# Kernel tuning notes

Measured on AMD Instinct MI355X. Metric: run time of the kernel, lower is better.

## Reference

```python
import jax, jax.numpy as jnp
import numpy as np

D = 1024
H = 16
B = 4
S = 2048
NEG = -1000000000.0


def setup_inputs() -> dict:
    key = jax.random.key(0)
    ks = jax.random.split(key, 12)
    s = 0.02
    inp = {
        "Q": jax.random.normal(ks[0], (B, S, D), jnp.float32),
        "K": jax.random.normal(ks[1], (B, S, D), jnp.float32),
        "V": jax.random.normal(ks[2], (B, S, D), jnp.float32),
        # causal mask, broadcastable to [B, H, S, S]
        "mask": jnp.broadcast_to(jnp.tril(jnp.ones((S, S), bool)), (B, 1, S, S)),
        "Wq": jax.random.normal(ks[3], (D, D), jnp.float32) * s,
        "bq": jnp.zeros((D,), jnp.float32),
        "Wk": jax.random.normal(ks[4], (D, D), jnp.float32) * s,
        "bk": jnp.zeros((D,), jnp.float32),
        "Wv": jax.random.normal(ks[5], (D, D), jnp.float32) * s,
        "bv": jnp.zeros((D,), jnp.float32),
        "Wo": jax.random.normal(ks[6], (D, D), jnp.float32) * s,
        "bo": jnp.zeros((D,), jnp.float32),
    }
    return inp


def reference(Q, K, V, mask, Wq, bq, Wk, bk, Wv, bv, Wo, bo):
    d = D // H  # head dim
    def split(x):  # [B,S,D] -> [B,H,S,d]
        Bx, Sx, _ = x.shape
        return x.reshape(Bx, Sx, H, d).transpose(0, 2, 1, 3)

    q = split(Q @ Wq + bq)
    k = split(K @ Wk + bk)
    v = split(V @ Wv + bv)

    scores = jnp.einsum("bhsd,bhtd->bhst", q, k) / jnp.sqrt(jnp.float32(d))
    scores = jnp.where(mask, scores, NEG)
    attn = jax.nn.softmax(scores, axis=-1)
    out = jnp.einsum("bhst,bhtd->bhsd", attn, v)  # [B,H,S,d]
    out = out.transpose(0, 2, 1, 3).reshape(Q.shape[0], Q.shape[1], D)
    return out @ Wo + bo
```

## Files before the change

kernel.cpp:

```cpp
#include <hip/hip_runtime.h>
#include <hip/hip_bf16.h>
#include <type_traits>

#define DEV __device__ __forceinline__

typedef short bf16x8 __attribute__((ext_vector_type(8)));
typedef float f32x4 __attribute__((ext_vector_type(4)));
typedef float f32x16 __attribute__((ext_vector_type(16)));
typedef unsigned u32x4 __attribute__((ext_vector_type(4)));

static DEV unsigned short f2bf(float f) {
  unsigned u = __builtin_bit_cast(unsigned, f);
  u += 0x7FFFu + ((u >> 16) & 1u);
  return (unsigned short)(u >> 16);
}

static DEV unsigned cvtpk(float lo, float hi) {
  unsigned d;
  asm("v_cvt_pk_bf16_f32 %0, %1, %2" : "=v"(d) : "v"(lo), "v"(hi));
  return d;
}

static DEV void pl32(unsigned& x, unsigned& y) {
  asm("v_permlane32_swap_b32 %0, %1" : "+v"(x), "+v"(y));
}

static DEV float vmax3(float a, float b, float c) {
  float d;
  asm("v_max3_f32 %0, %1, %2, %3" : "=v"(d) : "v"(a), "v"(b), "v"(c));
  return d;
}

static DEV void gl_lds16(const unsigned short* g, unsigned short* l) {
  __builtin_amdgcn_global_load_lds(
      (const __attribute__((address_space(1))) unsigned*)g,
      (__attribute__((address_space(3))) unsigned*)l, 16, 0, 0);
}

#define QSCALE 0.18033688f

__global__ __launch_bounds__(256) void wtrans4(const float* __restrict__ W0,
                                               const float* __restrict__ W1,
                                               const float* __restrict__ W2,
                                               const float* __restrict__ W3,
                                               unsigned short* __restrict__ T0,
                                               unsigned short* __restrict__ T1,
                                               unsigned short* __restrict__ T2,
                                               unsigned short* __restrict__ T3) {
  const int z = blockIdx.z;
  const float* W = z == 0 ? W0 : z == 1 ? W1 : z == 2 ? W2 : W3;
  unsigned short* Wt = z == 0 ? T0 : z == 1 ? T1 : z == 2 ? T2 : T3;
  const float wsc = (z == 0) ? QSCALE : 1.0f;
  __shared__ __align__(16) unsigned short T[64][72];
  const int tid = threadIdx.x;
  const int k0 = blockIdx.x * 64, n0 = blockIdx.y * 64;
  const int r = tid >> 4, c4 = (tid & 15) * 4;
  for (int j = 0; j < 4; ++j) {
    int row = j * 16 + r;
    float4 v = *(const float4*)&W[(size_t)(k0 + row) * 1024 + n0 + c4];
    ushort4 w;
    w.x = f2bf(v.x * wsc); w.y = f2bf(v.y * wsc);
    w.z = f2bf(v.z * wsc); w.w = f2bf(v.w * wsc);
    *(ushort4*)&T[row][c4] = w;
  }
  __syncthreads();
  for (int j = 0; j < 4; ++j) {
    int n = j * 16 + r;
    ushort4 w;
    w.x = T[c4 + 0][n]; w.y = T[c4 + 1][n]; w.z = T[c4 + 2][n]; w.w = T[c4 + 3][n];
    *(ushort4*)&Wt[(size_t)(n0 + n) * 1024 + k0 + c4] = w;
  }
}

__global__ __launch_bounds__(256) void xcvt3(const float* __restrict__ S0,
                                             const float* __restrict__ S1,
                                             const float* __restrict__ S2,
                                             unsigned short* __restrict__ D0,
                                             unsigned short* __restrict__ D1,
                                             unsigned short* __restrict__ D2) {
  const int z = blockIdx.z;
  const float* S = z == 0 ? S0 : z == 1 ? S1 : S2;
  unsigned short* D = z == 0 ? D0 : z == 1 ? D1 : D2;
  const size_t stride = (size_t)gridDim.x * 256 * 8;
  for (size_t i = ((size_t)blockIdx.x * 256 + threadIdx.x) * 8; i < 8u * 1024 * 1024;
       i += stride) {
    float4 a = *(const float4*)&S[i];
    float4 b = *(const float4*)&S[i + 4];
    uint4 w;
    w.x = cvtpk(a.x, a.y);
    w.y = cvtpk(a.z, a.w);
    w.z = cvtpk(b.x, b.y);
    w.w = cvtpk(b.z, b.w);
    *(uint4*)&D[i] = w;
  }
}

template <typename OutT>
DEV void gemm_lds_body(const unsigned short* __restrict__ X,
                       const unsigned short* __restrict__ Wt,
                       const float* __restrict__ bias, OutT* __restrict__ Y,
                       float bsc) {
  __shared__ __align__(16) unsigned short As[128 * 64];
  __shared__ __align__(16) unsigned short Bs[128 * 64];
  const int tid = threadIdx.x, lane = tid & 63, wid = tid >> 6;
  const int m0 = blockIdx.x * 128, n0 = blockIdx.y * 128;
  const int wm = (wid >> 1) * 64, wn = (wid & 1) * 64;
  f32x4 acc[4][4] = {};

  const int srow = wid * 32 + (lane >> 3);
  const int scol = (((lane & 7) ^ ((lane >> 3) & 7))) * 8;
  const unsigned short* gA = &X[(size_t)(m0 + srow) * 1024 + scol];
  const unsigned short* gB = &Wt[(size_t)(n0 + srow) * 1024 + scol];
  unsigned short* lA = &As[wid * 32 * 64];
  unsigned short* lB = &Bs[wid * 32 * 64];

  for (int k0 = 0; k0 < 1024; k0 += 64) {
    __syncthreads();
#pragma unroll
    for (int j = 0; j < 4; ++j) {
      gl_lds16(gA + (size_t)j * 8 * 1024 + k0, lA + j * 8 * 64);
      gl_lds16(gB + (size_t)j * 8 * 1024 + k0, lB + j * 8 * 64);
    }
    __syncthreads();
#pragma unroll
    for (int kk = 0; kk < 2; ++kk) {
      const int kb = ((kk * 4 + (lane >> 4)) ^ (lane & 7)) * 8;
      bf16x8 af[4], bfr[4];
#pragma unroll
      for (int i = 0; i < 4; ++i)
        af[i] = *(const bf16x8*)&As[(wm + i * 16 + (lane & 15)) * 64 + kb];
#pragma unroll
      for (int i = 0; i < 4; ++i)
        bfr[i] = *(const bf16x8*)&Bs[(wn + i * 16 + (lane & 15)) * 64 + kb];
      __builtin_amdgcn_s_setprio(1);
#pragma unroll
      for (int mi = 0; mi < 4; ++mi)
#pragma unroll
        for (int ni = 0; ni < 4; ++ni)
          acc[mi][ni] =
              __builtin_amdgcn_mfma_f32_16x16x32_bf16(af[mi], bfr[ni], acc[mi][ni], 0, 0, 0);
      __builtin_amdgcn_s_setprio(0);
    }
  }
  for (int ni = 0; ni < 4; ++ni) {
    const int col = n0 + wn + ni * 16 + (lane & 15);
    const float bv = bias[col] * bsc;
    for (int mi = 0; mi < 4; ++mi) {
      const int row = m0 + wm + mi * 16 + (lane >> 4) * 4;
      for (int r = 0; r < 4; ++r) {
        float v = acc[mi][ni][r] + bv;
        if constexpr (std::is_same_v<OutT, float>)
          Y[(size_t)(row + r) * 1024 + col] = v;
        else
          Y[(size_t)(row + r) * 1024 + col] = f2bf(v);
      }
    }
  }
}

__global__ __launch_bounds__(256) void gemm_qkv3(
    const unsigned short* __restrict__ X0, const unsigned short* __restrict__ X1,
    const unsigned short* __restrict__ X2, const unsigned short* __restrict__ W0,
    const unsigned short* __restrict__ W1, const unsigned short* __restrict__ W2,
    const float* __restrict__ b0, const float* __restrict__ b1,
    const float* __restrict__ b2, unsigned short* __restrict__ Y0,
    unsigned short* __restrict__ Y1, unsigned short* __restrict__ Y2) {
  const int z = blockIdx.z;
  const unsigned short* X = z == 0 ? X0 : z == 1 ? X1 : X2;
  const unsigned short* Wt = z == 0 ? W0 : z == 1 ? W1 : W2;
  const float* bias = z == 0 ? b0 : z == 1 ? b1 : b2;
  unsigned short* Y = z == 0 ? Y0 : z == 1 ? Y1 : Y2;
  gemm_lds_body<unsigned short>(X, Wt, bias, Y, z == 0 ? QSCALE : 1.0f);
}

__global__ __launch_bounds__(256) void gemm_out(const unsigned short* __restrict__ X,
                                                const unsigned short* __restrict__ Wt,
                                                const float* __restrict__ bias,
                                                float* __restrict__ Y) {
  gemm_lds_body<float>(X, Wt, bias, Y, 1.0f);
}

__global__ __launch_bounds__(256) void vtrans(const unsigned short* __restrict__ vbf,
                                              unsigned short* __restrict__ vt) {
  __shared__ __align__(16) unsigned short T[64][72];
  const int tid = threadIdx.x;
  const int s0 = blockIdx.x * 64;
  const int bh = blockIdx.y, b = bh >> 4, h = bh & 15;
  const int col0 = h * 64;
  const int rr = tid >> 3, c8 = (tid & 7) * 8;
  for (int p = 0; p < 2; ++p) {
    const int row = rr + 32 * p;
    *(uint4*)&T[row][c8] =
        *(const uint4*)&vbf[((size_t)b * 2048 + s0 + row) * 1024 + col0 + c8];
  }
  __syncthreads();
  const int dv = tid & 63, ss = (tid >> 6) * 16;
  union { uint4 v[2]; unsigned short s[16]; } o;
#pragma unroll
  for (int i = 0; i < 16; ++i) o.s[i] = T[ss + i][dv];
  *(uint4*)&vt[((size_t)bh * 64 + dv) * 2048 + s0 + ss] = o.v[0];
  *(uint4*)&vt[((size_t)bh * 64 + dv) * 2048 + s0 + ss + 8] = o.v[1];
}

__global__ __launch_bounds__(256) void attn_fwd(const unsigned short* __restrict__ Qb,
                                                const unsigned short* __restrict__ Kb,
                                                const unsigned short* __restrict__ Vt,
                                                unsigned short* __restrict__ Ob) {
  constexpr int KP = 72;
  __shared__ __align__(16) unsigned short SM[4 * 64 * KP];
  const int tid = threadIdx.x, lane = tid & 63, wid = tid >> 6;
  const int l31 = lane & 31, hi = lane >> 5;
  const int id = blockIdx.x;
  const int xcd = id & 7, idx = id >> 3;
  const int bh = xcd + 8 * (idx & 7);
  const int qb = idx >> 3;
  const int q0 = (15 - qb) * 128;
  const int b = bh >> 4, h = bh & 15;
  const size_t rowbase = (size_t)b * 2048;
  const int col0 = h * 64;
  const int qmin = q0 + wid * 32;
  const int myq = qmin + l31;
  const unsigned short* Vrow = Vt + (size_t)bh * 64 * 2048;
  const int rr = tid >> 3, c8 = (tid & 7) * 8;

  bf16x8 qf[4];
#pragma unroll
  for (int c = 0; c < 4; ++c)
    qf[c] = *(const bf16x8*)&Qb[(rowbase + myq) * 1024 + col0 + c * 16 + hi * 8];

  const bf16x8 onesv =
      __builtin_bit_cast(bf16x8, (u32x4){0x3F803F80u, 0x3F803F80u, 0x3F803F80u, 0x3F803F80u});

  f32x16 o[2], rsa;
  o[0] = 0.f; o[1] = 0.f; rsa = 0.f;
  float mrow = -1.0e30f;

  const int NT = q0 / 64 + 2;
  uint4 kr0, kr1, vr0, vr1;
#define LOADT(KV0)                                                              \
  do {                                                                          \
    const int _k = (KV0);                                                       \
    kr0 = *(const uint4*)&Kb[(rowbase + _k + rr) * 1024 + col0 + c8];           \
    kr1 = *(const uint4*)&Kb[(rowbase + _k + rr + 32) * 1024 + col0 + c8];      \
    vr0 = *(const uint4*)&Vrow[(size_t)rr * 2048 + _k + c8];                    \
    vr1 = *(const uint4*)&Vrow[(size_t)(rr + 32) * 2048 + _k + c8];             \
  } while (0)

  LOADT(0);
  {
    unsigned short* Ks = SM;
    unsigned short* Vs = SM + 64 * KP;
    *(uint4*)&Ks[rr * KP + c8] = kr0;
    *(uint4*)&Ks[(rr + 32) * KP + c8] = kr1;
    *(uint4*)&Vs[rr * KP + c8] = vr0;
    *(uint4*)&Vs[(rr + 32) * KP + c8] = vr1;
    LOADT(64);
    __syncthreads();
  }

  for (int t = 0; t < NT; ++t) {
    const int kv0 = t * 64;
    const int p = t & 1;
    if (kv0 <= qmin + 31) {
      const unsigned short* Ks = SM + p * 128 * KP;
      const unsigned short* Vs = Ks + 64 * KP;

      f32x16 s2[2];
      s2[0] = 0.f; s2[1] = 0.f;
      __builtin_amdgcn_s_setprio(1);
#pragma unroll
      for (int m = 0; m < 2; ++m)
#pragma unroll
        for (int c = 0; c < 4; ++c) {
          bf16x8 kf = *(const bf16x8*)&Ks[(m * 32 + l31) * KP + c * 16 + hi * 8];
          s2[m] = __builtin_amdgcn_mfma_f32_32x32x16_bf16(kf, qf[c], s2[m], 0, 0, 0);
        }
      __builtin_amdgcn_s_setprio(0);

      if (kv0 + 63 > qmin) {
        const int thr = l31 + (qmin - kv0);
#pragma unroll
        for (int m = 0; m < 2; ++m)
#pragma unroll
          for (int r = 0; r < 16; ++r) {
            const int kvl = m * 32 + (r & 3) + 8 * (r >> 2) + 4 * hi;
            if (kvl > thr) s2[m][r] = -1.0e30f;
          }
      }

      float tmax = fmaxf(s2[0][0], s2[0][1]);
#pragma unroll
      for (int m = 0; m < 2; ++m)
#pragma unroll
        for (int r = m == 0 ? 2 : 0; r < 16; r += 2)
          tmax = vmax3(tmax, s2[m][r], s2[m][r + 1]);
      tmax = fmaxf(tmax, __shfl_xor(tmax, 32));
      if (__any(tmax > mrow + 11.5f)) {
        const float mnew = fmaxf(mrow, tmax);
        const float al = __builtin_amdgcn_exp2f(mrow - mnew);
        mrow = mnew;
        o[0] *= al;
        o[1] *= al;
        rsa[0] *= al;
      }
#pragma unroll
      for (int m = 0; m < 2; ++m)
#pragma unroll
        for (int r = 0; r < 16; ++r)
          s2[m][r] = __builtin_amdgcn_exp2f(s2[m][r] - mrow);

      bf16x8 pf[4];
#pragma unroll
      for (int m = 0; m < 2; ++m) {
        unsigned a0 = cvtpk(s2[m][0], s2[m][1]), a1 = cvtpk(s2[m][2], s2[m][3]);
        unsigned b0 = cvtpk(s2[m][4], s2[m][5]), b1 = cvtpk(s2[m][6], s2[m][7]);
        pl32(a0, b0);
        pl32(a1, b1);
        pf[2 * m] = __builtin_bit_cast(bf16x8, (u32x4){a0, a1, b0, b1});
        unsigned c0 = cvtpk(s2[m][8], s2[m][9]), c1 = cvtpk(s2[m][10], s2[m][11]);
        unsigned d0 = cvtpk(s2[m][12], s2[m][13]), d1 = cvtpk(s2[m][14], s2[m][15]);
        pl32(c0, d0);
        pl32(c1, d1);
        pf[2 * m + 1] = __builtin_bit_cast(bf16x8, (u32x4){c0, c1, d0, d1});
      }

      __builtin_amdgcn_s_setprio(1);
#pragma unroll
      for (int nt = 0; nt < 2; ++nt)
#pragma unroll
        for (int cc = 0; cc < 4; ++cc) {
          bf16x8 vf = *(const bf16x8*)&Vs[(nt * 32 + l31) * KP + cc * 16 + hi * 8];
          o[nt] = __builtin_amdgcn_mfma_f32_32x32x16_bf16(vf, pf[cc], o[nt], 0, 0, 0);
        }
#pragma unroll
      for (int cc = 0; cc < 4; ++cc)
        rsa = __builtin_amdgcn_mfma_f32_32x32x16_bf16(onesv, pf[cc], rsa, 0, 0, 0);
      __builtin_amdgcn_s_setprio(0);
    }
    if (t + 1 < NT) {
      unsigned short* Ks = SM + (p ^ 1) * 128 * KP;
      unsigned short* Vs = Ks + 64 * KP;
      *(uint4*)&Ks[rr * KP + c8] = kr0;
      *(uint4*)&Ks[(rr + 32) * KP + c8] = kr1;
      *(uint4*)&Vs[rr * KP + c8] = vr0;
      *(uint4*)&Vs[(rr + 32) * KP + c8] = vr1;
      if (t + 2 < NT) LOADT(kv0 + 128);
    }
    __syncthreads();
  }
#undef LOADT

  unsigned short* Os = SM + wid * 32 * KP;
  const float inv = 1.0f / rsa[0];
#pragma unroll
  for (int nt = 0; nt < 2; ++nt)
#pragma unroll
    for (int rq = 0; rq < 4; ++rq)
#pragma unroll
      for (int j = 0; j < 2; ++j) {
        const int r = rq * 4 + 2 * j;
        const unsigned pk = cvtpk(o[nt][r] * inv, o[nt][r + 1] * inv);
        *(unsigned*)&Os[l31 * KP + nt * 32 + 8 * rq + 4 * hi + 2 * j] = pk;
      }
  __syncthreads();
#pragma unroll
  for (int i = 0; i < 4; ++i) {
    const int qq = (lane >> 3) + i * 8;
    const int dvc = (lane & 7) * 8;
    uint4 val = *(const uint4*)&Os[qq * KP + dvc];
    *(uint4*)&Ob[(rowbase + qmin + qq) * 1024 + col0 + dvc] = val;
  }
}

extern "C" void kernel_launch(void* const* d_in, const int* in_sizes, int n_in,
                              void* d_out, int out_size, void* d_ws, size_t ws_size,
                              hipStream_t stream) {
  const float* Q  = (const float*)d_in[0];
  const float* K  = (const float*)d_in[1];
  const float* V  = (const float*)d_in[2];
  const float* Wq = (const float*)d_in[4];
  const float* bq = (const float*)d_in[5];
  const float* Wk = (const float*)d_in[6];
  const float* bk = (const float*)d_in[7];
  const float* Wv = (const float*)d_in[8];
  const float* bv = (const float*)d_in[9];
  const float* Wo = (const float*)d_in[10];
  const float* bo = (const float*)d_in[11];
  float* out = (float*)d_out;

  const size_t MB = 1024 * 1024;
  char* ws = (char*)d_ws;
  unsigned short* qb  = (unsigned short*)(ws + 0 * MB);
  unsigned short* kb  = (unsigned short*)(ws + 16 * MB);
  unsigned short* vbf = (unsigned short*)(ws + 32 * MB);
  unsigned short* vt  = (unsigned short*)(ws + 48 * MB);
  unsigned short* wtq = (unsigned short*)(ws + 64 * MB);
  unsigned short* wtk = (unsigned short*)(ws + 66 * MB);
  unsigned short* wtv = (unsigned short*)(ws + 68 * MB);
  unsigned short* wto = (unsigned short*)(ws + 70 * MB);
  unsigned short* ob  = vbf;

  wtrans4<<<dim3(16, 16, 4), 256, 0, stream>>>(Wq, Wk, Wv, Wo, wtq, wtk, wtv, wto);

  if (ws_size >= 120 * MB) {
    unsigned short* qx = (unsigned short*)(ws + 72 * MB);
    unsigned short* kx = (unsigned short*)(ws + 88 * MB);
    unsigned short* vx = (unsigned short*)(ws + 104 * MB);
    xcvt3<<<dim3(2048, 1, 3), 256, 0, stream>>>(Q, K, V, qx, kx, vx);
    gemm_qkv3<<<dim3(64, 8, 3), 256, 0, stream>>>(qx, kx, vx, wtq, wtk, wtv,
                                                  bq, bk, bv, qb, kb, vbf);
  } else {
    unsigned short* xb = vt;
    const float* Xs[3] = {Q, K, V};
    const unsigned short* Ws[3] = {wtq, wtk, wtv};
    const float* Bs[3] = {bq, bk, bv};
    unsigned short* Ys[3] = {qb, kb, vbf};
    for (int t = 0; t < 3; ++t) {
      xcvt3<<<dim3(2048, 1, 1), 256, 0, stream>>>(Xs[t], Xs[t], Xs[t], xb, xb, xb);
      gemm_qkv3<<<dim3(64, 8, 1), 256, 0, stream>>>(xb, xb, xb, Ws[t], Ws[t], Ws[t],
                                                    Bs[t], Bs[t], Bs[t],
                                                    Ys[t], Ys[t], Ys[t]);
    }
  }

  vtrans<<<dim3(32, 64), 256, 0, stream>>>(vbf, vt);

  attn_fwd<<<1024, 256, 0, stream>>>(qb, kb, vt, ob);

  gemm_out<<<dim3(64, 8), 256, 0, stream>>>(ob, wto, bo, out);
}
```

Before: 200.4 us.

## Fuse V transpose into QKV GEMM epilogue and drop vtrans kernel

The V projection GEMM now writes its output directly in the per-head transposed layout [B,H,d,S] through an LDS-staged epilogue, so the separate vtrans kernel and its extra 16MB read and write of V are gone. The Q and K paths keep the row-major epilogue. The workspace is rearranged so the attention output gets its own buffer, and the fallback path passes a z offset. The V epilogue adds extra barriers and LDS round trips inside the GEMM blocks.

```diff
diff --git a/kernel.cpp b/kernel.cpp
--- a/kernel.cpp
+++ b/kernel.cpp
@@ -95,13 +95,14 @@
   }
 }
 
-template <typename OutT>
+template <typename OutT, bool TRANSV>
 DEV void gemm_lds_body(const unsigned short* __restrict__ X,
                        const unsigned short* __restrict__ Wt,
                        const float* __restrict__ bias, OutT* __restrict__ Y,
                        float bsc) {
-  __shared__ __align__(16) unsigned short As[128 * 64];
-  __shared__ __align__(16) unsigned short Bs[128 * 64];
+  __shared__ __align__(16) unsigned short SMG[2 * 128 * 64];
+  unsigned short* As = SMG;
+  unsigned short* Bs = SMG + 128 * 64;
   const int tid = threadIdx.x, lane = tid & 63, wid = tid >> 6;
   const int m0 = blockIdx.x * 128, n0 = blockIdx.y * 128;
   const int wm = (wid >> 1) * 64, wn = (wid & 1) * 64;
@@ -142,17 +143,55 @@
       __builtin_amdgcn_s_setprio(0);
     }
   }
-  for (int ni = 0; ni < 4; ++ni) {
-    const int col = n0 + wn + ni * 16 + (lane & 15);
-    const float bv = bias[col] * bsc;
-    for (int mi = 0; mi < 4; ++mi) {
-      const int row = m0 + wm + mi * 16 + (lane >> 4) * 4;
-      for (int r = 0; r < 4; ++r) {
-        float v = acc[mi][ni][r] + bv;
-        if constexpr (std::is_same_v<OutT, float>)
-          Y[(size_t)(row + r) * 1024 + col] = v;
-        else
-          Y[(size_t)(row + r) * 1024 + col] = f2bf(v);
+
+  if constexpr (TRANSV) {
+    const int bt = m0 >> 11;
+    const int s0 = m0 & 2047;
+    const int h0 = n0 >> 6;
+    unsigned short* Tl = SMG;
+#pragma unroll
+    for (int cch = 0; cch < 2; ++cch) {
+      __syncthreads();
+      if ((wid >> 1) == cch) {
+#pragma unroll
+        for (int ni = 0; ni < 4; ++ni) {
+          const int n = wn + ni * 16 + (lane & 15);
+          const float bv = bias[n0 + n] * bsc;
+#pragma unroll
+          for (int mi = 0; mi < 4; ++mi) {
+            const int mloc = mi * 16 + (lane >> 4) * 4;
+#pragma unroll
+            for (int r = 0; r < 4; r += 2) {
+              const unsigned pk = cvtpk(acc[mi][ni][r] + bv, acc[mi][ni][r + 1] + bv);
+              *(unsigned*)&Tl[n * 72 + mloc + r] = pk;
+            }
+          }
+        }
+      }
+      __syncthreads();
+      const int m8 = (tid & 7) * 8;
+#pragma unroll
+      for (int it = 0; it < 4; ++it) {
+        const int nr = (tid >> 3) + it * 32;
+        const int h = h0 + (nr >> 6), dv = nr & 63;
+        uint4 v = *(const uint4*)&Tl[nr * 72 + m8];
+        *(uint4*)&((unsigned short*)Y)[(((size_t)bt * 16 + h) * 64 + dv) * 2048 +
+                                       s0 + cch * 64 + m8] = v;
+      }
+    }
+  } else {
+    for (int ni = 0; ni < 4; ++ni) {
+      const int col = n0 + wn + ni * 16 + (lane & 15);
+      const float bv = bias[col] * bsc;
+      for (int mi = 0; mi < 4; ++mi) {
+        const int row = m0 + wm + mi * 16 + (lane >> 4) * 4;
+        for (int r = 0; r < 4; ++r) {
+          float v = acc[mi][ni][r] + bv;
+          if constexpr (std::is_same_v<OutT, float>)
+            Y[(size_t)(row + r) * 1024 + col] = v;
+          else
+            Y[(size_t)(row + r) * 1024 + col] = f2bf(v);
+        }
       }
     }
   }
@@ -164,42 +203,23 @@
     const unsigned short* __restrict__ W1, const unsigned short* __restrict__ W2,
     const float* __restrict__ b0, const float* __restrict__ b1,
     const float* __restrict__ b2, unsigned short* __restrict__ Y0,
-    unsigned short* __restrict__ Y1, unsigned short* __restrict__ Y2) {
-  const int z = blockIdx.z;
+    unsigned short* __restrict__ Y1, unsigned short* __restrict__ Y2, int zoff) {
+  const int z = blockIdx.z + zoff;
   const unsigned short* X = z == 0 ? X0 : z == 1 ? X1 : X2;
   const unsigned short* Wt = z == 0 ? W0 : z == 1 ? W1 : W2;
   const float* bias = z == 0 ? b0 : z == 1 ? b1 : b2;
   unsigned short* Y = z == 0 ? Y0 : z == 1 ? Y1 : Y2;
-  gemm_lds_body<unsigned short>(X, Wt, bias, Y, z == 0 ? QSCALE : 1.0f);
+  if (z == 2)
+    gemm_lds_body<unsigned short, true>(X, Wt, bias, Y, 1.0f);
+  else
+    gemm_lds_body<unsigned short, false>(X, Wt, bias, Y, z == 0 ? QSCALE : 1.0f);
 }
 
 __global__ __launch_bounds__(256) void gemm_out(const unsigned short* __restrict__ X,
                                                 const unsigned short* __restrict__ Wt,
                                                 const float* __restrict__ bias,
                                                 float* __restrict__ Y) {
-  gemm_lds_body<float>(X, Wt, bias, Y, 1.0f);
-}
-
-__global__ __launch_bounds__(256) void vtrans(const unsigned short* __restrict__ vbf,
-                                              unsigned short* __restrict__ vt) {
-  __shared__ __align__(16) unsigned short T[64][72];
-  const int tid = threadIdx.x;
-  const int s0 = blockIdx.x * 64;
-  const int bh = blockIdx.y, b = bh >> 4, h = bh & 15;
-  const int col0 = h * 64;
-  const int rr = tid >> 3, c8 = (tid & 7) * 8;
-  for (int p = 0; p < 2; ++p) {
-    const int row = rr + 32 * p;
-    *(uint4*)&T[row][c8] =
-        *(const uint4*)&vbf[((size_t)b * 2048 + s0 + row) * 1024 + col0 + c8];
-  }
-  __syncthreads();
-  const int dv = tid & 63, ss = (tid >> 6) * 16;
-  union { uint4 v[2]; unsigned short s[16]; } o;
-#pragma unroll
-  for (int i = 0; i < 16; ++i) o.s[i] = T[ss + i][dv];
-  *(uint4*)&vt[((size_t)bh * 64 + dv) * 2048 + s0 + ss] = o.v[0];
-  *(uint4*)&vt[((size_t)bh * 64 + dv) * 2048 + s0 + ss + 8] = o.v[1];
+  gemm_lds_body<float, false>(X, Wt, bias, Y, 1.0f);
 }
 
 __global__ __launch_bounds__(256) void attn_fwd(const unsigned short* __restrict__ Qb,
@@ -392,13 +412,12 @@
   char* ws = (char*)d_ws;
   unsigned short* qb  = (unsigned short*)(ws + 0 * MB);
   unsigned short* kb  = (unsigned short*)(ws + 16 * MB);
-  unsigned short* vbf = (unsigned short*)(ws + 32 * MB);
-  unsigned short* vt  = (unsigned short*)(ws + 48 * MB);
+  unsigned short* vtB = (unsigned short*)(ws + 32 * MB);
+  unsigned short* ob  = (unsigned short*)(ws + 48 * MB);
   unsigned short* wtq = (unsigned short*)(ws + 64 * MB);
   unsigned short* wtk = (unsigned short*)(ws + 66 * MB);
   unsigned short* wtv = (unsigned short*)(ws + 68 * MB);
   unsigned short* wto = (unsigned short*)(ws + 70 * MB);
-  unsigned short* ob  = vbf;
 
   wtrans4<<<dim3(16, 16, 4), 256, 0, stream>>>(Wq, Wk, Wv, Wo, wtq, wtk, wtv, wto);
 
@@ -408,24 +427,18 @@
     unsigned short* vx = (unsigned short*)(ws + 104 * MB);
     xcvt3<<<dim3(2048, 1, 3), 256, 0, stream>>>(Q, K, V, qx, kx, vx);
     gemm_qkv3<<<dim3(64, 8, 3), 256, 0, stream>>>(qx, kx, vx, wtq, wtk, wtv,
-                                                  bq, bk, bv, qb, kb, vbf);
+                                                  bq, bk, bv, qb, kb, vtB, 0);
   } else {
-    unsigned short* xb = vt;
+    unsigned short* xb = ob;
     const float* Xs[3] = {Q, K, V};
-    const unsigned short* Ws[3] = {wtq, wtk, wtv};
-    const float* Bs[3] = {bq, bk, bv};
-    unsigned short* Ys[3] = {qb, kb, vbf};
     for (int t = 0; t < 3; ++t) {
       xcvt3<<<dim3(2048, 1, 1), 256, 0, stream>>>(Xs[t], Xs[t], Xs[t], xb, xb, xb);
-      gemm_qkv3<<<dim3(64, 8, 1), 256, 0, stream>>>(xb, xb, xb, Ws[t], Ws[t], Ws[t],
-                                                    Bs[t], Bs[t], Bs[t],
-                                                    Ys[t], Ys[t], Ys[t]);
-    }
-  }
-
-  vtrans<<<dim3(32, 64), 256, 0, stream>>>(vbf, vt);
-
-  attn_fwd<<<1024, 256, 0, stream>>>(qb, kb, vt, ob);
+      gemm_qkv3<<<dim3(64, 8, 1), 256, 0, stream>>>(xb, xb, xb, wtq, wtk, wtv,
+                                                    bq, bk, bv, qb, kb, vtB, t);
+    }
+  }
+
+  attn_fwd<<<1024, 256, 0, stream>>>(qb, kb, vtB, ob);
 
   gemm_out<<<dim3(64, 8), 256, 0, stream>>>(ob, wto, bo, out);
 }
```

Result: faster. 186.3 us (-7.0%).
